# Performance work log

Hardware: AMD Instinct MI355X
Metric: run time of the kernel (lower is better)

Reference implementation:

```python
import jax, jax.numpy as jnp
import numpy as np

KS = 3  # deformable kernel size

def conv2d(x, w, pad, stride=1):
    return jax.lax.conv_general_dilated(
        x, w, (stride, stride), [(pad, pad), (pad, pad)],
        dimension_numbers=('NCHW', 'OIHW', 'NCHW'))

def deform_conv(x, wp, bp, wc):
    # Faithful port of DeformConv2d(inc, outc, kernel_size=3, padding=1, stride=1)
    b, c, h, w = x.shape
    N = KS * KS
    offset = conv2d(x, wp, 1) + bp[None, :, None, None]  # [b, 2N, h, w]
    xpad = jnp.pad(x, ((0, 0), (0, 0), (1, 1), (1, 1)))
    Hp, Wp = h + 2, w + 2
    # p_n: kernel-relative offsets (x coords first, then y coords)
    rng = jnp.arange(-(KS - 1) // 2, (KS - 1) // 2 + 1, dtype=x.dtype)
    pnx, pny = jnp.meshgrid(rng, rng, indexing='ij')
    p_n = jnp.concatenate([pnx.reshape(-1), pny.reshape(-1)])  # [2N]
    # p_0: base sampling grid (1-indexed into padded map)
    p0x = jnp.broadcast_to(jnp.arange(1, h + 1, dtype=x.dtype)[:, None], (h, w))
    p0y = jnp.broadcast_to(jnp.arange(1, w + 1, dtype=x.dtype)[None, :], (h, w))
    p0 = jnp.concatenate([jnp.broadcast_to(p0x, (N, h, w)),
                          jnp.broadcast_to(p0y, (N, h, w))], 0)  # [2N,h,w]
    p = p0[None] + p_n[None, :, None, None] + offset  # [b,2N,h,w]
    p = jnp.transpose(p, (0, 2, 3, 1))  # [b,h,w,2N]
    qf = jax.lax.stop_gradient(jnp.floor(p))
    qltx = jnp.clip(qf[..., :N], 0, Hp - 1)
    qlty = jnp.clip(qf[..., N:], 0, Wp - 1)
    qrbx = jnp.clip(qf[..., :N] + 1, 0, Hp - 1)
    qrby = jnp.clip(qf[..., N:] + 1, 0, Wp - 1)
    px = jnp.clip(p[..., :N], 0, Hp - 1)
    py = jnp.clip(p[..., N:], 0, Wp - 1)
    g_lt = (1 + (qltx - px)) * (1 + (qlty - py))
    g_rb = (1 - (qrbx - px)) * (1 - (qrby - py))
    g_lb = (1 + (qltx - px)) * (1 - (qrby - py))
    g_rt = (1 - (qrbx - px)) * (1 + (qlty - py))
    xflat = xpad.reshape(b, c, Hp * Wp)
    def gather(qx, qy):
        idx = (qx.astype(jnp.int32) * Wp + qy.astype(jnp.int32)).reshape(b, 1, -1)
        idx = jnp.broadcast_to(idx, (b, c, idx.shape[-1]))
        return jnp.take_along_axis(xflat, idx, axis=2).reshape(b, c, h, w, N)
    xo = (g_lt[:, None] * gather(qltx, qlty) + g_rb[:, None] * gather(qrbx, qrby)
          + g_lb[:, None] * gather(qltx, qrby) + g_rt[:, None] * gather(qrbx, qlty))
    # rearrange 'b c h w (i j) -> b c (h i) (w j)'
    xo = xo.reshape(b, c, h, w, KS, KS).transpose(0, 1, 2, 4, 3, 5).reshape(b, c, h * KS, w * KS)
    return conv2d(xo, wc, 1, stride=KS)


def setup_inputs() -> dict:
    key = jax.random.key(0)
    B, C, H, W = 4, 64, 256, 256
    DIM, S0 = 64, 5
    ks = jax.random.split(key, 14)
    s = 0.02
    inp = {
        'x': jax.random.normal(ks[0], (B, C, H, W), jnp.float32),
        'wp_a': jax.random.normal(ks[1], (2 * KS * KS, C, 3, 3), jnp.float32) * s,
        'bp_a': jnp.zeros((2 * KS * KS,), jnp.float32),
        'wc_a': jax.random.normal(ks[2], (C, C, KS, KS), jnp.float32) * s,
        'w1_a': jax.random.normal(ks[3], (C, C, 1, 1), jnp.float32) * s,
        'b1_a': jax.random.normal(ks[4], (C,), jnp.float32) * s,
        'wp_p': jax.random.normal(ks[5], (2 * KS * KS, C, 3, 3), jnp.float32) * s,
        'bp_p': jnp.zeros((2 * KS * KS,), jnp.float32),
        'wc_p': jax.random.normal(ks[6], (C, C, KS, KS), jnp.float32) * s,
        'w1_p': jax.random.normal(ks[7], (C, C, 1, 1), jnp.float32) * s,
        'b1_p': jax.random.normal(ks[8], (C,), jnp.float32) * s,
        'w0': jax.random.normal(ks[9], (DIM, C, S0, S0), jnp.float32) * s,
        'b0': jax.random.normal(ks[10], (DIM,), jnp.float32) * s,
    }
    return inp


def reference(x, wp_a, bp_a, wc_a, w1_a, b1_a, wp_p, bp_p, wc_p, w1_p, b1_p, w0, b0):
    H, W = x.shape[2], x.shape[3]
    xf = jnp.fft.rfft2(x, axes=(2, 3))
    amp = jnp.abs(xf)
    pha = jnp.angle(xf)
    amp3 = deform_conv(amp, wp_a, bp_a, wc_a)
    amp1 = conv2d(amp, w1_a, 0) + b1_a[None, :, None, None]
    pha3 = deform_conv(pha, wp_p, bp_p, wc_p)
    pha1 = conv2d(pha, w1_p, 0) + b1_p[None, :, None, None]
    eps = 1e-08
    real_13 = amp1 * jnp.cos(pha3) + eps
    imag_31 = amp3 * jnp.sin(pha1) + eps
    real_31 = amp3 * jnp.cos(pha1) + eps
    imag_13 = amp1 * jnp.sin(pha3) + eps
    out_c = (real_13 + real_31) + 1j * (imag_31 + imag_13) + eps
    xr = jnp.abs(jnp.fft.irfft2(out_c, s=(H, W), axes=(2, 3)))
    s0 = w0.shape[2]
    return conv2d(xr, w0, s0 // 2) + b0[None, :, None, None]
```

## Files before the change

### kernel.cpp

```cpp
#include <hip/hip_runtime.h>
#include <math.h>

#define BB 4
#define CC 64
#define HH 256
#define WW 256
#define WF 129
#define NPIX (WF*HH)
#define NS ((size_t)BB*CC*NPIX)
#define TWOPI 6.283185307179586f

typedef __attribute__((ext_vector_type(8))) short short8v;
typedef __attribute__((ext_vector_type(4))) float float4v;

__device__ __forceinline__ float2 cmulf(float2 a, float2 b) {
    return make_float2(a.x*b.x - a.y*b.y, a.x*b.y + a.y*b.x);
}

template<int SIGN>
__device__ __forceinline__ float2 fft256_lds(const float2* __restrict__ xs,
                                             float2* __restrict__ ys,
                                             const float2* __restrict__ tw,
                                             const float2* __restrict__ tw16,
                                             int t) {
    int k1 = t & 15, n2 = t >> 4;
    float2 acc = make_float2(0.f, 0.f);
    #pragma unroll
    for (int n1 = 0; n1 < 16; ++n1) {
        float2 v = xs[n1*16 + n2];
        float2 w = tw16[(n1*k1) & 15];
        float ws = (SIGN < 0) ? -w.y : w.y;
        acc.x = fmaf(v.x, w.x, fmaf(-v.y, ws, acc.x));
        acc.y = fmaf(v.x, ws, fmaf( v.y, w.x, acc.y));
    }
    float2 w2 = tw[n2*k1];
    float w2s = (SIGN < 0) ? -w2.y : w2.y;
    ys[t] = cmulf(acc, make_float2(w2.x, w2s));
    __syncthreads();
    float2 acc2 = make_float2(0.f, 0.f);
    #pragma unroll
    for (int m2 = 0; m2 < 16; ++m2) {
        float2 v = ys[m2*16 + k1];
        float2 w = tw16[(m2*n2) & 15];
        float ws = (SIGN < 0) ? -w.y : w.y;
        acc2.x = fmaf(v.x, w.x, fmaf(-v.y, ws, acc2.x));
        acc2.y = fmaf(v.x, ws, fmaf( v.y, w.x, acc2.y));
    }
    return acc2;
}

__global__ void k_tw(float2* __restrict__ twg) {
    int m = threadIdx.x;
    float s, c;
    sincosf((TWOPI/256.f) * (float)m, &s, &c);
    twg[m] = make_float2(c, s);
}

__global__ __launch_bounds__(256) void k_fft_rows(const float* __restrict__ x,
                                                  const float2* __restrict__ twg,
                                                  float* __restrict__ r1re,
                                                  float* __restrict__ r1im) {
    __shared__ float2 xs[256], ys[256];
    __shared__ float2 tw[256];
    __shared__ float2 tw16[16];
    int t = threadIdx.x;
    int bid = blockIdx.x;
    int y = bid & 255;
    int bc = bid >> 8;
    tw[t] = twg[t];
    if (t < 16) tw16[t] = twg[t*16];
    xs[t] = make_float2(x[(size_t)bc*HH*WW + (size_t)y*WW + t], 0.f);
    __syncthreads();
    float2 X = fft256_lds<-1>(xs, ys, tw, tw16, t);
    if (t < WF) {
        r1re[((size_t)bc*WF + t)*HH + y] = X.x;
        r1im[((size_t)bc*WF + t)*HH + y] = X.y;
    }
}

__global__ __launch_bounds__(256) void k_fft_cols(const float* __restrict__ r1re,
                                                  const float* __restrict__ r1im,
                                                  const float2* __restrict__ twg,
                                                  float* __restrict__ amp,
                                                  float* __restrict__ pha) {
    __shared__ float2 xs[256], ys[256];
    __shared__ float2 tw[256];
    __shared__ float2 tw16[16];
    int t = threadIdx.x;
    int bid = blockIdx.x;
    int k = bid % WF;
    int bc = bid / WF;
    size_t base = ((size_t)bc*WF + k)*HH;
    tw[t] = twg[t];
    if (t < 16) tw16[t] = twg[t*16];
    xs[t] = make_float2(r1re[base + t], r1im[base + t]);
    __syncthreads();
    float2 X = fft256_lds<-1>(xs, ys, tw, tw16, t);
    amp[base + t] = sqrtf(X.x*X.x + X.y*X.y);
    pha[base + t] = atan2f(X.y, X.x);
}

__global__ __launch_bounds__(256) void k_pack(const float* __restrict__ src,
                                              float* __restrict__ dst) {
    __shared__ float tile[64][65];
    int tid = threadIdx.x;
    int bid = blockIdx.x;
    int it = bid & 3;
    int rest = bid >> 2;
    int k = rest % WF;
    int b = rest / WF;
    int i0 = it*64;
    int ii = tid & 63;
    int cg = tid >> 6;
    for (int rep = 0; rep < 16; ++rep) {
        int c = cg*16 + rep;
        tile[c][ii] = src[(size_t)(b*CC + c)*NPIX + (size_t)k*HH + i0 + ii];
    }
    __syncthreads();
    for (int rep = 0; rep < 16; ++rep) {
        int m = cg*16 + rep;
        dst[((size_t)(b*WF + k)*HH + i0 + m)*CC + ii] = tile[ii][m];
    }
}

__device__ __forceinline__ unsigned short bf16r(float f) {
    unsigned u = __float_as_uint(f);
    unsigned r = (u + 0x7FFFu + ((u >> 16) & 1u)) >> 16;
    return (unsigned short)r;
}
__device__ __forceinline__ float bf16f(unsigned short h) {
    return __uint_as_float(((unsigned)h) << 16);
}

__global__ void k_wct(const float* __restrict__ wc,
                      unsigned short* __restrict__ wh,
                      unsigned short* __restrict__ wl) {
    int idx = blockIdx.x*256 + threadIdx.x;
    if (idx < 64*576) {
        int k = idx % 576;
        int oc = idx / 576;
        int pos = k >> 6;
        int c = k & 63;
        float v = wc[((size_t)oc*64 + c)*9 + pos];
        unsigned short h = bf16r(v);
        wh[idx] = h;
        wl[idx] = bf16r(v - bf16f(h));
    }
}

__global__ void k_wsplit(const float* __restrict__ w0,
                         unsigned short* __restrict__ whT,
                         unsigned short* __restrict__ wlT) {
    int idx = blockIdx.x*256 + threadIdx.x;
    if (idx < 25*64*64) {
        int c = idx & 63;
        int t = idx >> 6;
        int oc = t & 63;
        int tap = t >> 6;
        float v = w0[((size_t)oc*CC + c)*25 + tap];
        unsigned short h = bf16r(v);
        float l = v - bf16f(h);
        whT[idx] = h;
        wlT[idx] = bf16r(l);
    }
}

__global__ void k_wpt(const float* __restrict__ wpa, const float* __restrict__ wpp,
                      float* __restrict__ wta, float* __restrict__ wtp) {
    int idx = blockIdx.x*256 + threadIdx.x;
    if (idx < 64*162) {
        int c = idx / 162;
        int r = idx - c*162;
        int oc = r / 9, pos = r - oc*9;
        size_t s = ((size_t)oc*CC + c)*9 + pos;
        wta[idx] = wpa[s];
        wtp[idx] = wpp[s];
    }
}

__global__ __launch_bounds__(256) void k_off2(const float* __restrict__ amp,
                                              const float* __restrict__ pha,
                                              const float* __restrict__ wptA,
                                              const float* __restrict__ wptP,
                                              const float* __restrict__ bpA,
                                              const float* __restrict__ bpP,
                                              float* __restrict__ offa,
                                              float* __restrict__ offp) {
    __shared__ float colb[2][3][260];
    int tid = threadIdx.x;
    int bid = blockIdx.x;
    int sel = (bid >= BB*WF) ? 1 : 0;
    int rb = sel ? bid - BB*WF : bid;
    int j = rb % WF;
    int b = rb / WF;
    const float* img = sel ? pha : amp;
    const float* wpt = sel ? wptP : wptA;
    const float* bp  = sel ? bpP  : bpA;
    float* off = sel ? offp : offa;

    const float* ib = img + (size_t)b*CC*NPIX + (size_t)j*HH;
    bool jm = (j > 0), jp = (j < WF-1);

    float acc[18];
    #pragma unroll
    for (int o = 0; o < 18; ++o) acc[o] = bp[o];

    if (tid < 12) {
        int bufi = tid & 1;
        int dj = (tid >> 1) % 3;
        int e = tid / 6;
        colb[bufi][dj][e ? 257 : 0] = 0.f;
    }
    {
        const float* cb = ib;
        colb[0][1][tid+1] = cb[tid];
        colb[0][0][tid+1] = jm ? cb[tid - HH] : 0.f;
        colb[0][2][tid+1] = jp ? cb[tid + HH] : 0.f;
    }
    __syncthreads();

    for (int c = 0; c < CC; ++c) {
        int cur = c & 1;
        if (c + 1 < CC) {
            const float* cb = ib + (size_t)(c+1)*NPIX;
            colb[cur^1][1][tid+1] = cb[tid];
            colb[cur^1][0][tid+1] = jm ? cb[tid - HH] : 0.f;
            colb[cur^1][2][tid+1] = jp ? cb[tid + HH] : 0.f;
        }
        float v[9];
        #pragma unroll
        for (int di = 0; di < 3; ++di)
            #pragma unroll
            for (int dj = 0; dj < 3; ++dj)
                v[di*3+dj] = colb[cur][dj][tid + di];
        const float* wc = wpt + c*162;
        #pragma unroll
        for (int o = 0; o < 18; ++o) {
            #pragma unroll
            for (int p = 0; p < 9; ++p)
                acc[o] = fmaf(wc[o*9+p], v[p], acc[o]);
        }
        __syncthreads();
    }

    size_t ob = ((size_t)(b*18)*WF + j)*HH + tid;
    #pragma unroll
    for (int o = 0; o < 18; ++o)
        off[ob + (size_t)o*WF*HH] = acc[o];
}

#define SPAD 328
__global__ __launch_bounds__(256) void k_deform(const float* __restrict__ imgc,
                                                const float* __restrict__ off,
                                                const unsigned short* __restrict__ wh,
                                                const unsigned short* __restrict__ wl,
                                                float* __restrict__ out) {
    __shared__ int   cidx[4][144];
    __shared__ float cwgt[4][144];
    __shared__ __align__(16) unsigned short Sh[16][SPAD];
    __shared__ __align__(16) unsigned short Sl[16][SPAD];
    int tid = threadIdx.x;
    int bid = blockIdx.x;
    int it = bid & 15;
    int rest = bid >> 4;
    int j = rest % WF;
    int b = rest / WF;
    int i0 = it * 16;

    if (tid < 144) {
        int pix = tid / 9;
        int pos = tid % 9;
        int ki = pos / 3, kj = pos % 3;
        int i = i0 + pix;
        int r = 3*i + ki - 1;
        int s = 3*j + kj - 1;
        float g[4] = {0.f,0.f,0.f,0.f};
        int ix[4] = {-1,-1,-1,-1};
        if (r >= 0 && s >= 0) {
            int hq = r/3, nx = r%3;
            int wq = s/3, ny = s%3;
            int n = nx*3 + ny;
            float ox = off[((size_t)(b*18 + n)*WF + wq)*HH + hq];
            float oy = off[((size_t)(b*18 + 9 + n)*WF + wq)*HH + hq];
            float pxf = (float)(hq + nx) + ox;
            float pyf = (float)(wq + ny) + oy;
            float qx = floorf(pxf), qy = floorf(pyf);
            float qltx = fminf(fmaxf(qx, 0.f), 257.f);
            float qlty = fminf(fmaxf(qy, 0.f), 130.f);
            float qrbx = fminf(fmaxf(qx + 1.f, 0.f), 257.f);
            float qrby = fminf(fmaxf(qy + 1.f, 0.f), 130.f);
            float pxc = fminf(fmaxf(pxf, 0.f), 257.f);
            float pyc = fminf(fmaxf(pyf, 0.f), 130.f);
            float glt = (1.f + (qltx - pxc)) * (1.f + (qlty - pyc));
            float grb = (1.f - (qrbx - pxc)) * (1.f - (qrby - pyc));
            float glb = (1.f + (qltx - pxc)) * (1.f - (qrby - pyc));
            float grt = (1.f - (qrbx - pxc)) * (1.f + (qlty - pyc));
            int ax0 = (int)qltx, ax1 = (int)qrbx;
            int ay0 = (int)qlty, ay1 = (int)qrby;
            int cx[4] = {ax0, ax1, ax0, ax1};
            int cy[4] = {ay0, ay1, ay1, ay0};
            g[0]=glt; g[1]=grb; g[2]=glb; g[3]=grt;
            #pragma unroll
            for (int q = 0; q < 4; ++q) {
                int a = cx[q], bq = cy[q];
                ix[q] = (a >= 1 && a <= 256 && bq >= 1 && bq <= 129)
                        ? ((bq-1)*HH + (a-1))*CC : -1;
            }
        }
        #pragma unroll
        for (int q = 0; q < 4; ++q) { cidx[q][tid] = ix[q]; cwgt[q][tid] = g[q]; }
    }
    __syncthreads();

    const float* cb = imgc + (size_t)b * (size_t)WF * HH * CC;
    int lane = tid & 63;
    int w = tid >> 6;
    int l15 = lane & 15;
    int l4 = lane >> 4;
    float4v acc = {0.f, 0.f, 0.f, 0.f};
    const unsigned short* wbh = wh + (size_t)(w*16 + l15)*576 + l4*8;
    const unsigned short* wbl = wl + (size_t)(w*16 + l15)*576 + l4*8;

    for (int t = tid; t < 4096; t += 256) {
        int c = t & 63;
        int s = t >> 6;
        int pix = s >> 2, pos = s & 3;
        int combo = pix*9 + pos;
        float sum = 0.f;
        #pragma unroll
        for (int q = 0; q < 4; ++q) {
            int ofs = cidx[q][combo];
            float v = (ofs >= 0) ? cb[(size_t)ofs + c] : 0.f;
            sum += cwgt[q][combo] * v;
        }
        unsigned short h = bf16r(sum);
        Sh[pix][pos*64 + c] = h;
        Sl[pix][pos*64 + c] = bf16r(sum - bf16f(h));
    }
    __syncthreads();
    #pragma unroll
    for (int k0 = 0; k0 < 256; k0 += 32) {
        short8v Ah = *(const short8v*)&wbh[k0];
        short8v Al = *(const short8v*)&wbl[k0];
        short8v Bh = *(const short8v*)&Sh[l15][k0 + l4*8];
        short8v Bl = *(const short8v*)&Sl[l15][k0 + l4*8];
        acc = __builtin_amdgcn_mfma_f32_16x16x32_bf16(Ah, Bh, acc, 0, 0, 0);
        acc = __builtin_amdgcn_mfma_f32_16x16x32_bf16(Ah, Bl, acc, 0, 0, 0);
        acc = __builtin_amdgcn_mfma_f32_16x16x32_bf16(Al, Bh, acc, 0, 0, 0);
    }
    __syncthreads();

    for (int t = tid; t < 5120; t += 256) {
        int c = t & 63;
        int s = t >> 6;
        int pix = s / 5, pp = s - pix*5;
        int combo = pix*9 + 4 + pp;
        float sum = 0.f;
        #pragma unroll
        for (int q = 0; q < 4; ++q) {
            int ofs = cidx[q][combo];
            float v = (ofs >= 0) ? cb[(size_t)ofs + c] : 0.f;
            sum += cwgt[q][combo] * v;
        }
        unsigned short h = bf16r(sum);
        Sh[pix][pp*64 + c] = h;
        Sl[pix][pp*64 + c] = bf16r(sum - bf16f(h));
    }
    __syncthreads();
    #pragma unroll
    for (int k0 = 0; k0 < 320; k0 += 32) {
        short8v Ah = *(const short8v*)&wbh[256 + k0];
        short8v Al = *(const short8v*)&wbl[256 + k0];
        short8v Bh = *(const short8v*)&Sh[l15][k0 + l4*8];
        short8v Bl = *(const short8v*)&Sl[l15][k0 + l4*8];
        acc = __builtin_amdgcn_mfma_f32_16x16x32_bf16(Ah, Bh, acc, 0, 0, 0);
        acc = __builtin_amdgcn_mfma_f32_16x16x32_bf16(Ah, Bl, acc, 0, 0, 0);
        acc = __builtin_amdgcn_mfma_f32_16x16x32_bf16(Al, Bh, acc, 0, 0, 0);
    }

    size_t ob = (size_t)b*CC*NPIX + (size_t)j*HH + i0;
    #pragma unroll
    for (int r = 0; r < 4; ++r) {
        int oc = w*16 + l4*4 + r;
        out[ob + (size_t)oc*NPIX + l15] = acc[r];
    }
}

__global__ __launch_bounds__(256) void k_combine(const float* __restrict__ ampc,
                                                 const float* __restrict__ phac,
                                                 float* __restrict__ a3,
                                                 float* __restrict__ p3,
                                                 const float* __restrict__ w1a,
                                                 const float* __restrict__ b1a,
                                                 const float* __restrict__ w1p,
                                                 const float* __restrict__ b1p) {
    __shared__ float la[64][65], lp[64][65];
    int tid = threadIdx.x;
    int bid = blockIdx.x;
    int quarter = bid & 3;
    int rest = bid >> 2;
    int j = rest % WF;
    int b = rest / WF;
    int i0 = quarter * 64;
    size_t gbase = ((size_t)(b*WF + j)*HH + i0) * CC;
    for (int rep = 0; rep < 16; ++rep) {
        int t = rep*256 + tid;
        int pix = t >> 6;
        int c = t & 63;
        la[c][pix] = ampc[gbase + t];
        lp[c][pix] = phac[gbase + t];
    }
    __syncthreads();
    int ii = tid & 63;
    int wv = tid >> 6;
    float acc_a[16], acc_p[16];
    #pragma unroll
    for (int q = 0; q < 16; ++q) { acc_a[q] = b1a[wv*16+q]; acc_p[q] = b1p[wv*16+q]; }
    for (int c = 0; c < CC; ++c) {
        float av = la[c][ii], pv = lp[c][ii];
        #pragma unroll
        for (int q = 0; q < 16; ++q) {
            acc_a[q] += w1a[(wv*16+q)*CC + c] * av;
            acc_p[q] += w1p[(wv*16+q)*CC + c] * pv;
        }
    }
    #pragma unroll
    for (int q = 0; q < 16; ++q) {
        int oc = wv*16 + q;
        size_t idx = (size_t)(b*CC + oc)*NPIX + (size_t)j*HH + i0 + ii;
        float a3v = a3[idx];
        float p3v = p3[idx];
        float s1, c1, s3, c3;
        sincosf(acc_p[q], &s1, &c1);
        sincosf(p3v, &s3, &c3);
        float re = acc_a[q]*c3 + a3v*c1 + 3e-8f;
        float im = a3v*s1 + acc_a[q]*s3 + 2e-8f;
        a3[idx] = re;
        p3[idx] = im;
    }
}

__global__ __launch_bounds__(256) void k_ifft_cols(const float* __restrict__ ocre,
                                                   const float* __restrict__ ocim,
                                                   const float2* __restrict__ twg,
                                                   float* __restrict__ r2re,
                                                   float* __restrict__ r2im) {
    __shared__ float2 xs[256], ys[256];
    __shared__ float2 tw[256];
    __shared__ float2 tw16[16];
    int t = threadIdx.x;
    int bid = blockIdx.x;
    int k = bid % WF;
    int bc = bid / WF;
    size_t base = ((size_t)bc*WF + k)*HH;
    tw[t] = twg[t];
    if (t < 16) tw16[t] = twg[t*16];
    xs[t] = make_float2(ocre[base + t], ocim[base + t]);
    __syncthreads();
    float2 X = fft256_lds<1>(xs, ys, tw, tw16, t);
    size_t ob = ((size_t)bc*HH + t)*WF + k;
    r2re[ob] = X.x * (1.0f/256.0f);
    r2im[ob] = X.y * (1.0f/256.0f);
}

__global__ __launch_bounds__(256) void k_irfft_rows(const float* __restrict__ r2re,
                                                    const float* __restrict__ r2im,
                                                    const float2* __restrict__ twg,
                                                    float* __restrict__ xr) {
    __shared__ float2 xs[256], ys[256];
    __shared__ float2 tw[256];
    __shared__ float2 tw16[16];
    int t = threadIdx.x;
    int bid = blockIdx.x;
    int y = bid & 255;
    int bc = bid >> 8;
    size_t base = ((size_t)bc*HH + y)*WF;
    tw[t] = twg[t];
    if (t < 16) tw16[t] = twg[t*16];
    if (t < WF) xs[t] = make_float2(r2re[base + t], r2im[base + t]);
    __syncthreads();
    if (t >= WF) {
        float2 v = xs[256 - t];
        xs[t] = make_float2(v.x, -v.y);
    }
    __syncthreads();
    float2 X = fft256_lds<1>(xs, ys, tw, tw16, t);
    xr[((size_t)bc*HH + y)*WW + t] = fabsf(X.x * (1.0f/256.0f));
}

__global__ __launch_bounds__(256) void k_split(const float* __restrict__ xr,
                                               unsigned short* __restrict__ xh,
                                               unsigned short* __restrict__ xl) {
    __shared__ float tile[64][65];
    int tid = threadIdx.x;
    int bid = blockIdx.x;
    int q = bid & 3;
    int y = (bid >> 2) & 255;
    int b = bid >> 10;
    int x0 = q*64;
    int lane = tid & 63;
    int cg = tid >> 6;
    for (int rep = 0; rep < 16; ++rep) {
        int c = cg*16 + rep;
        tile[c][lane] = xr[(((size_t)(b*CC + c)*HH + y)*WW) + x0 + lane];
    }
    __syncthreads();
    int x = tid >> 2;
    int c0 = (tid & 3)*8;
    #pragma unroll
    for (int ch = 0; ch < 2; ++ch) {
        short8v hv, lv;
        #pragma unroll
        for (int j = 0; j < 8; ++j) {
            float v = tile[ch*32 + c0 + j][x];
            unsigned short h = bf16r(v);
            float l = v - bf16f(h);
            hv[j] = (short)h;
            lv[j] = (short)bf16r(l);
        }
        size_t ob = ((((size_t)(b*2 + ch)*HH + y)*WW) + x0 + x)*32 + c0;
        *(short8v*)&xh[ob] = hv;
        *(short8v*)&xl[ob] = lv;
    }
}

#define LROW 40
#define LX 72
#define LROWS 6
#define PLANE (LROWS*LX*LROW)
#define NSLOT 7

__global__ __launch_bounds__(256) void k_conv5m(const unsigned short* __restrict__ xh,
                                                const unsigned short* __restrict__ xl,
                                                const unsigned short* __restrict__ whT,
                                                const unsigned short* __restrict__ wlT,
                                                const float* __restrict__ b0,
                                                float* __restrict__ out) {
    __shared__ unsigned short smem[2*PLANE];
    int tid = threadIdx.x;
    int bid = blockIdx.x;
    int q = bid & 3;
    int yb = (bid >> 2) & 127;
    int b = bid >> 9;
    int x0 = q*64;
    int y0 = yb*2;
    int lane = tid & 63;
    int w = tid >> 6;
    int wrow = w >> 1;
    int oc0 = (w & 1)*32;
    int l15 = lane & 15;
    int l4  = lane >> 4;

    int goff[NSLOT], loff[NSLOT];
    bool inb[NSLOT], okimg[NSLOT];
    #pragma unroll
    for (int s = 0; s < NSLOT; ++s) {
        int it = tid + s*256;
        int part = it & 3;
        int idx = it >> 2;
        int row = idx / LX;
        int xi = idx - row*LX;
        int gy = y0 + row - 2;
        int gx = x0 + xi - 2;
        bool ib = (it < LROWS*LX*4);
        bool ok = ib && gy >= 0 && gy < HH && gx >= 0 && gx < WW;
        inb[s] = ib;
        okimg[s] = ok;
        goff[s] = ok ? ((gy*WW + gx)*32 + part*8) : 0;
        loff[s] = ib ? ((row*LX + xi)*LROW + part*8) : 0;
    }

    float4v acc[2][4];
    #pragma unroll
    for (int o = 0; o < 2; ++o) {
        float4v bi;
        #pragma unroll
        for (int r = 0; r < 4; ++r) bi[r] = b0[oc0 + o*16 + l4*4 + r];
        #pragma unroll
        for (int p = 0; p < 4; ++p) acc[o][p] = bi;
    }

    short8v rh[NSLOT], rl[NSLOT];
    const short8v zero8 = {0,0,0,0,0,0,0,0};

#define PREFETCH(CH) do { \
        size_t chb = ((size_t)(b*2 + (CH)) << 16) * 32; \
        _Pragma("unroll") \
        for (int s = 0; s < NSLOT; ++s) { \
            rh[s] = *(const short8v*)&xh[chb + goff[s]]; \
            rl[s] = *(const short8v*)&xl[chb + goff[s]]; \
        } \
    } while (0)

#define WRITE() do { \
        _Pragma("unroll") \
        for (int s = 0; s < NSLOT; ++s) { \
            if (inb[s]) { \
                *(short8v*)&smem[loff[s]]         = okimg[s] ? rh[s] : zero8; \
                *(short8v*)&smem[PLANE + loff[s]] = okimg[s] ? rl[s] : zero8; \
            } \
        } \
    } while (0)

#define LOADA(TAP, CH, A0, A1, A2, A3r) do { \
        size_t wb = ((size_t)(TAP)*64 + oc0 + l15)*64 + (size_t)(CH)*32 + l4*8; \
        A0  = *(const short8v*)&whT[wb]; \
        A1  = *(const short8v*)&whT[wb + 1024]; \
        A2  = *(const short8v*)&wlT[wb]; \
        A3r = *(const short8v*)&wlT[wb + 1024]; \
    } while (0)

#define LOADB(TAP, B_h, B_l) do { \
        int dy = (TAP)/5, dx = (TAP) - dy*5; \
        int rbase = (wrow + dy)*LX + l15 + dx; \
        _Pragma("unroll") \
        for (int p = 0; p < 4; ++p) { \
            int a = (rbase + p*16)*LROW + l4*8; \
            B_h[p] = *(const short8v*)&smem[a]; \
            B_l[p] = *(const short8v*)&smem[a + PLANE]; \
        } \
    } while (0)

#define MFMAS(A0, A1, A2, A3r, B_h, B_l) do { \
        _Pragma("unroll") for (int p = 0; p < 4; ++p) \
            acc[0][p] = __builtin_amdgcn_mfma_f32_16x16x32_bf16(A0, B_h[p], acc[0][p], 0, 0, 0); \
        _Pragma("unroll") for (int p = 0; p < 4; ++p) \
            acc[1][p] = __builtin_amdgcn_mfma_f32_16x16x32_bf16(A1, B_h[p], acc[1][p], 0, 0, 0); \
        _Pragma("unroll") for (int p = 0; p < 4; ++p) \
            acc[0][p] = __builtin_amdgcn_mfma_f32_16x16x32_bf16(A0, B_l[p], acc[0][p], 0, 0, 0); \
        _Pragma("unroll") for (int p = 0; p < 4; ++p) \
            acc[1][p] = __builtin_amdgcn_mfma_f32_16x16x32_bf16(A1, B_l[p], acc[1][p], 0, 0, 0); \
        _Pragma("unroll") for (int p = 0; p < 4; ++p) \
            acc[0][p] = __builtin_amdgcn_mfma_f32_16x16x32_bf16(A2, B_h[p], acc[0][p], 0, 0, 0); \
        _Pragma("unroll") for (int p = 0; p < 4; ++p) \
            acc[1][p] = __builtin_amdgcn_mfma_f32_16x16x32_bf16(A3r, B_h[p], acc[1][p], 0, 0, 0); \
    } while (0)

#define COMPUTE(CH) do { \
        short8v cA0, cA1, cA2, cA3, nA0, nA1, nA2, nA3; \
        short8v cBh[4], cBl[4]; \
        LOADA(0, CH, cA0, cA1, cA2, cA3); \
        _Pragma("unroll 5") \
        for (int tap = 0; tap < 25; ++tap) { \
            if (tap < 24) LOADA(tap+1, CH, nA0, nA1, nA2, nA3); \
            LOADB(tap, cBh, cBl); \
            MFMAS(cA0, cA1, cA2, cA3, cBh, cBl); \
            if (tap < 24) { cA0 = nA0; cA1 = nA1; cA2 = nA2; cA3 = nA3; } \
        } \
    } while (0)

    PREFETCH(0);
    WRITE();
    __syncthreads();
    PREFETCH(1);
    COMPUTE(0);
    __syncthreads();
    WRITE();
    __syncthreads();
    COMPUTE(1);

#undef PREFETCH
#undef WRITE
#undef LOADA
#undef LOADB
#undef MFMAS
#undef COMPUTE

    int y = y0 + wrow;
    #pragma unroll
    for (int o = 0; o < 2; ++o) {
        #pragma unroll
        for (int p = 0; p < 4; ++p) {
            #pragma unroll
            for (int r = 0; r < 4; ++r) {
                int oc = oc0 + o*16 + l4*4 + r;
                int x = x0 + p*16 + l15;
                out[(((size_t)(b*CC + oc)*HH + y)*WW) + x] = acc[o][p][r];
            }
        }
    }
}

extern "C" void kernel_launch(void* const* d_in, const int* in_sizes, int n_in,
                              void* d_out, int out_size, void* d_ws, size_t ws_size,
                              hipStream_t stream) {
    const float* x    = (const float*)d_in[0];
    const float* wp_a = (const float*)d_in[1];
    const float* bp_a = (const float*)d_in[2];
    const float* wc_a = (const float*)d_in[3];
    const float* w1_a = (const float*)d_in[4];
    const float* b1_a = (const float*)d_in[5];
    const float* wp_p = (const float*)d_in[6];
    const float* bp_p = (const float*)d_in[7];
    const float* wc_p = (const float*)d_in[8];
    const float* w1_p = (const float*)d_in[9];
    const float* b1_p = (const float*)d_in[10];
    const float* w0   = (const float*)d_in[11];
    const float* b0   = (const float*)d_in[12];
    float* out = (float*)d_out;
    float* ws  = (float*)d_ws;

    float* R0 = ws;
    float* R1 = ws + 2*NS;
    float* R2 = ws + 4*NS;

    float* r1re = R0;
    float* r1im = R0 + NS;
    float* amp  = R1;
    float* pha  = R1 + NS;
    float* ampc = R0;
    float* phac = R0 + NS;
    size_t offsz = (size_t)BB*18*NPIX;
    float* offa = R2;
    float* offp = R2 + offsz;
    unsigned short* wsp = (unsigned short*)(R2 + 2*offsz);
    unsigned short* whA = wsp;
    unsigned short* wlA = wsp + 36864;
    unsigned short* whP = wsp + 2*36864;
    unsigned short* wlP = wsp + 3*36864;
    unsigned short* whT = wsp + 4*36864;
    unsigned short* wlT = whT + 25*64*64;
    float* wptA = (float*)(wlT + 25*64*64);
    float* wptP = wptA + 64*162;
    float2* twg = (float2*)(wptP + 64*162);
    float* A3   = R1;
    float* P3   = R1 + NS;
    float* r2re = R0;
    float* r2im = R0 + NS;
    float* xrp  = R1;
    unsigned short* xhp = (unsigned short*)R0;
    unsigned short* xlp = xhp + (size_t)BB*2*HH*WW*32;

    k_tw<<<1, 256, 0, stream>>>(twg);
    k_wct<<<144, 256, 0, stream>>>(wc_a, whA, wlA);
    k_wct<<<144, 256, 0, stream>>>(wc_p, whP, wlP);
    k_wsplit<<<400, 256, 0, stream>>>(w0, whT, wlT);
    k_wpt<<<41, 256, 0, stream>>>(wp_a, wp_p, wptA, wptP);
    k_fft_rows<<<BB*CC*HH, 256, 0, stream>>>(x, twg, r1re, r1im);
    k_fft_cols<<<BB*CC*WF, 256, 0, stream>>>(r1re, r1im, twg, amp, pha);
    k_pack<<<BB*WF*4, 256, 0, stream>>>(amp, ampc);
    k_pack<<<BB*WF*4, 256, 0, stream>>>(pha, phac);
    k_off2<<<2*BB*WF, 256, 0, stream>>>(amp, pha, wptA, wptP, bp_a, bp_p, offa, offp);
    k_deform<<<BB*WF*16, 256, 0, stream>>>(ampc, offa, whA, wlA, A3);
    k_deform<<<BB*WF*16, 256, 0, stream>>>(phac, offp, whP, wlP, P3);
    k_combine<<<BB*WF*4, 256, 0, stream>>>(ampc, phac, A3, P3, w1_a, b1_a, w1_p, b1_p);
    k_ifft_cols<<<BB*CC*WF, 256, 0, stream>>>(A3, P3, twg, r2re, r2im);
    k_irfft_rows<<<BB*CC*HH, 256, 0, stream>>>(r2re, r2im, twg, xrp);
    k_split<<<BB*HH*4, 256, 0, stream>>>(xrp, xhp, xlp);
    k_conv5m<<<BB*128*4, 256, 0, stream>>>(xhp, xlp, whT, wlT, b0, out);
}
```

Baseline: 1.598 ms.

## Batch 16 rows per block in row FFTs and vectorize transposed stores

The forward row FFT and inverse row FFT kernels now each process 16 rows per block using an in-place LDS FFT. The transposed intermediate accesses become float4 writes and reads of 16 consecutive y values instead of scattered scalar accesses. The inverse column FFT now writes its output in column-major layout (k,y) so the batched row kernel can read it with vector loads. This targets uncoalesced strided global traffic and per-block twiddle setup, at the cost of 32KB of LDS per block, more registers for 16 results, and fewer blocks in flight.

Result: slower. 2.208 ms (+38.2%).

```diff
diff --git a/kernel.cpp b/kernel.cpp
--- a/kernel.cpp
+++ b/kernel.cpp
@@ -49,6 +49,39 @@
     return acc2;
 }
 
+template<int SIGN>
+__device__ __forceinline__ float2 fft256_ip(float2* __restrict__ buf,
+                                            const float2* __restrict__ tw,
+                                            const float2* __restrict__ tw16,
+                                            int t) {
+    int k1 = t & 15, n2 = t >> 4;
+    float2 acc = make_float2(0.f, 0.f);
+    #pragma unroll
+    for (int n1 = 0; n1 < 16; ++n1) {
+        float2 v = buf[n1*16 + n2];
+        float2 w = tw16[(n1*k1) & 15];
+        float ws = (SIGN < 0) ? -w.y : w.y;
+        acc.x = fmaf(v.x, w.x, fmaf(-v.y, ws, acc.x));
+        acc.y = fmaf(v.x, ws, fmaf( v.y, w.x, acc.y));
+    }
+    float2 w2 = tw[n2*k1];
+    float w2s = (SIGN < 0) ? -w2.y : w2.y;
+    float2 mid = cmulf(acc, make_float2(w2.x, w2s));
+    __syncthreads();
+    buf[t] = mid;
+    __syncthreads();
+    float2 acc2 = make_float2(0.f, 0.f);
+    #pragma unroll
+    for (int m2 = 0; m2 < 16; ++m2) {
+        float2 v = buf[m2*16 + k1];
+        float2 w = tw16[(m2*n2) & 15];
+        float ws = (SIGN < 0) ? -w.y : w.y;
+        acc2.x = fmaf(v.x, w.x, fmaf(-v.y, ws, acc2.x));
+        acc2.y = fmaf(v.x, ws, fmaf( v.y, w.x, acc2.y));
+    }
+    return acc2;
+}
+
 __global__ void k_tw(float2* __restrict__ twg) {
     int m = threadIdx.x;
     float s, c;
@@ -60,21 +93,34 @@
                                                   const float2* __restrict__ twg,
                                                   float* __restrict__ r1re,
                                                   float* __restrict__ r1im) {
-    __shared__ float2 xs[256], ys[256];
+    __shared__ float2 buf[16][256];
     __shared__ float2 tw[256];
     __shared__ float2 tw16[16];
     int t = threadIdx.x;
     int bid = blockIdx.x;
-    int y = bid & 255;
-    int bc = bid >> 8;
+    int yt = bid & 15;
+    int bc = bid >> 4;
+    int y0 = yt*16;
     tw[t] = twg[t];
     if (t < 16) tw16[t] = twg[t*16];
-    xs[t] = make_float2(x[(size_t)bc*HH*WW + (size_t)y*WW + t], 0.f);
-    __syncthreads();
-    float2 X = fft256_lds<-1>(xs, ys, tw, tw16, t);
+    const float* xb = x + (size_t)bc*HH*WW + (size_t)y0*WW;
+    #pragma unroll
+    for (int r = 0; r < 16; ++r)
+        buf[r][t] = make_float2(xb[r*WW + t], 0.f);
+    __syncthreads();
+    float2 res[16];
+    #pragma unroll
+    for (int r = 0; r < 16; ++r)
+        res[r] = fft256_ip<-1>(buf[r], tw, tw16, t);
     if (t < WF) {
-        r1re[((size_t)bc*WF + t)*HH + y] = X.x;
-        r1im[((size_t)bc*WF + t)*HH + y] = X.y;
+        size_t base = ((size_t)bc*WF + t)*HH + y0;
+        #pragma unroll
+        for (int g = 0; g < 4; ++g) {
+            float4 vr = make_float4(res[g*4].x, res[g*4+1].x, res[g*4+2].x, res[g*4+3].x);
+            float4 vi = make_float4(res[g*4].y, res[g*4+1].y, res[g*4+2].y, res[g*4+3].y);
+            *(float4*)&r1re[base + g*4] = vr;
+            *(float4*)&r1im[base + g*4] = vi;
+        }
     }
 }
 
@@ -458,34 +504,51 @@
     xs[t] = make_float2(ocre[base + t], ocim[base + t]);
     __syncthreads();
     float2 X = fft256_lds<1>(xs, ys, tw, tw16, t);
-    size_t ob = ((size_t)bc*HH + t)*WF + k;
-    r2re[ob] = X.x * (1.0f/256.0f);
-    r2im[ob] = X.y * (1.0f/256.0f);
+    r2re[base + t] = X.x * (1.0f/256.0f);
+    r2im[base + t] = X.y * (1.0f/256.0f);
 }
 
 __global__ __launch_bounds__(256) void k_irfft_rows(const float* __restrict__ r2re,
                                                     const float* __restrict__ r2im,
                                                     const float2* __restrict__ twg,
                                                     float* __restrict__ xr) {
-    __shared__ float2 xs[256], ys[256];
+    __shared__ float2 buf[16][256];
     __shared__ float2 tw[256];
     __shared__ float2 tw16[16];
     int t = threadIdx.x;
     int bid = blockIdx.x;
-    int y = bid & 255;
-    int bc = bid >> 8;
-    size_t base = ((size_t)bc*HH + y)*WF;
+    int yt = bid & 15;
+    int bc = bid >> 4;
+    int y0 = yt*16;
     tw[t] = twg[t];
     if (t < 16) tw16[t] = twg[t*16];
-    if (t < WF) xs[t] = make_float2(r2re[base + t], r2im[base + t]);
+    if (t < WF) {
+        size_t base = ((size_t)bc*WF + t)*HH + y0;
+        #pragma unroll
+        for (int g = 0; g < 4; ++g) {
+            float4 vr = *(const float4*)&r2re[base + g*4];
+            float4 vi = *(const float4*)&r2im[base + g*4];
+            buf[g*4+0][t] = make_float2(vr.x, vi.x);
+            buf[g*4+1][t] = make_float2(vr.y, vi.y);
+            buf[g*4+2][t] = make_float2(vr.z, vi.z);
+            buf[g*4+3][t] = make_float2(vr.w, vi.w);
+        }
+    }
     __syncthreads();
     if (t >= WF) {
-        float2 v = xs[256 - t];
-        xs[t] = make_float2(v.x, -v.y);
-    }
-    __syncthreads();
-    float2 X = fft256_lds<1>(xs, ys, tw, tw16, t);
-    xr[((size_t)bc*HH + y)*WW + t] = fabsf(X.x * (1.0f/256.0f));
+        #pragma unroll
+        for (int r = 0; r < 16; ++r) {
+            float2 v = buf[r][256 - t];
+            buf[r][t] = make_float2(v.x, -v.y);
+        }
+    }
+    __syncthreads();
+    float* xb = xr + (size_t)bc*HH*WW + (size_t)y0*WW;
+    #pragma unroll
+    for (int r = 0; r < 16; ++r) {
+        float2 X = fft256_ip<1>(buf[r], tw, tw16, t);
+        xb[r*WW + t] = fabsf(X.x * (1.0f/256.0f));
+    }
 }
 
 __global__ __launch_bounds__(256) void k_split(const float* __restrict__ xr,
@@ -736,7 +799,7 @@
     k_wct<<<144, 256, 0, stream>>>(wc_p, whP, wlP);
     k_wsplit<<<400, 256, 0, stream>>>(w0, whT, wlT);
     k_wpt<<<41, 256, 0, stream>>>(wp_a, wp_p, wptA, wptP);
-    k_fft_rows<<<BB*CC*HH, 256, 0, stream>>>(x, twg, r1re, r1im);
+    k_fft_rows<<<BB*CC*16, 256, 0, stream>>>(x, twg, r1re, r1im);
     k_fft_cols<<<BB*CC*WF, 256, 0, stream>>>(r1re, r1im, twg, amp, pha);
     k_pack<<<BB*WF*4, 256, 0, stream>>>(amp, ampc);
     k_pack<<<BB*WF*4, 256, 0, stream>>>(pha, phac);
@@ -745,7 +808,7 @@
     k_deform<<<BB*WF*16, 256, 0, stream>>>(phac, offp, whP, wlP, P3);
     k_combine<<<BB*WF*4, 256, 0, stream>>>(ampc, phac, A3, P3, w1_a, b1_a, w1_p, b1_p);
     k_ifft_cols<<<BB*CC*WF, 256, 0, stream>>>(A3, P3, twg, r2re, r2im);
-    k_irfft_rows<<<BB*CC*HH, 256, 0, stream>>>(r2re, r2im, twg, xrp);
+    k_irfft_rows<<<BB*CC*16, 256, 0, stream>>>(r2re, r2im, twg, xrp);
     k_split<<<BB*HH*4, 256, 0, stream>>>(xrp, xhp, xlp);
     k_conv5m<<<BB*128*4, 256, 0, stream>>>(xhp, xlp, whT, wlT, b0, out);
 }
```
